# Kernel tuning notes

Measured on AMD Instinct MI355X. Metric: run time of the kernel, lower is better.

## Reference

```python
import jax, jax.numpy as jnp
import numpy as np

EPS = 1e-5

@jax.custom_vjp
def ste_quantize(w):
    # abs-mean scale, round, clamp to {-1, 0, 1}
    scale = jnp.maximum(jnp.mean(jnp.abs(w)), EPS)
    return jnp.clip(jnp.round(w / scale), -1.0, 1.0)

def _ste_fwd(w):
    return ste_quantize(w), None

def _ste_bwd(_, g):
    # straight-through: gradient passes unchanged
    return (g,)

ste_quantize.defvjp(_ste_fwd, _ste_bwd)


def setup_inputs() -> dict:
    key = jax.random.key(0)
    k1, k2 = jax.random.split(key)
    x = jax.random.normal(k1, (8, 8192, 1024), dtype=jnp.float32)       # [B, S, in]
    weight = jax.random.normal(k2, (1024, 1024), dtype=jnp.float32) * 0.02  # [out, in]
    return {"x": x, "weight": weight}


def reference(x, weight):
    w_ternary = ste_quantize(weight)                         # [out, in] in {-1,0,1}
    scale = jnp.maximum(jnp.mean(jnp.abs(weight)), EPS)      # scalar (differentiable path)
    # F.linear(x, w_ternary * scale): out = x @ (w_ternary*scale)^T
    return jnp.einsum('bsi,oi->bso', x, w_ternary * scale)
```

## Files before the change

### kernel.cpp

```cpp
#include <hip/hip_runtime.h>
#include <stdint.h>

#define K_DIM 1024
#define N_DIM 1024
#define M_MAX 65536

#define BM 256
#define BN 256
#define BK 32
#define NKT (K_DIM / BK)
#define NBUF 3
#define A_TILE (BM * BK)
#define B_TILE (BN * BK)

typedef __attribute__((ext_vector_type(8))) __bf16 bf16x8;
typedef __attribute__((ext_vector_type(4))) float f32x4;

__device__ __align__(16) unsigned short g_wq[N_DIM * K_DIM];
__device__ __align__(16) unsigned short g_xq[(size_t)M_MAX * K_DIM];
__device__ double g_partial[256];
__device__ float g_scale;

__device__ __forceinline__ unsigned int pack_bf16(float hi, float lo) {
  return __builtin_amdgcn_perm(__float_as_uint(hi), __float_as_uint(lo), 0x07060302u);
}

__global__ void absum_kernel(const float* __restrict__ w) {
  const int tid = threadIdx.x, bid = blockIdx.x;
  const float4* w4 = (const float4*)w;
  double s = 0.0;
#pragma unroll
  for (int i = 0; i < 4; i++) {
    float4 v = w4[bid * 1024 + i * 256 + tid];
    s += (double)fabsf(v.x) + (double)fabsf(v.y) + (double)fabsf(v.z) + (double)fabsf(v.w);
  }
#pragma unroll
  for (int o = 32; o > 0; o >>= 1) s += __shfl_down(s, o);
  __shared__ double sm[4];
  if ((tid & 63) == 0) sm[tid >> 6] = s;
  __syncthreads();
  if (tid == 0) g_partial[bid] = sm[0] + sm[1] + sm[2] + sm[3];
}

__global__ void scale_kernel() {
  const int tid = threadIdx.x;
  double v = g_partial[tid];
#pragma unroll
  for (int o = 32; o > 0; o >>= 1) v += __shfl_down(v, o);
  __shared__ double sm[4];
  if ((tid & 63) == 0) sm[tid >> 6] = v;
  __syncthreads();
  if (tid == 0) {
    double total = sm[0] + sm[1] + sm[2] + sm[3];
    double mean = total * (1.0 / 1048576.0);
    g_scale = (float)fmax(mean, 1e-5);
  }
}

__global__ void quant_kernel(const float* __restrict__ w) {
  const int idx = blockIdx.x * 256 + threadIdx.x;
  const float s = g_scale;
  float4 v = ((const float4*)w)[idx];
  float q0 = fminf(1.f, fmaxf(-1.f, rintf(v.x / s)));
  float q1 = fminf(1.f, fmaxf(-1.f, rintf(v.y / s)));
  float q2 = fminf(1.f, fmaxf(-1.f, rintf(v.z / s)));
  float q3 = fminf(1.f, fmaxf(-1.f, rintf(v.w / s)));
  ushort4 o;
  o.x = (unsigned short)(__float_as_uint(q0) >> 16);
  o.y = (unsigned short)(__float_as_uint(q1) >> 16);
  o.z = (unsigned short)(__float_as_uint(q2) >> 16);
  o.w = (unsigned short)(__float_as_uint(q3) >> 16);
  ((ushort4*)g_wq)[idx] = o;
}

__global__ __launch_bounds__(256) void convert_x(const float* __restrict__ x) {
  const size_t t = (size_t)blockIdx.x * 256 + threadIdx.x;
  const float4* x4 = (const float4*)x;
  float4 a = x4[t * 2];
  float4 b = x4[t * 2 + 1];
  uint4 o;
  o.x = pack_bf16(a.y, a.x);
  o.y = pack_bf16(a.w, a.z);
  o.z = pack_bf16(b.y, b.x);
  o.w = pack_bf16(b.w, b.z);
  ((uint4*)g_xq)[t] = o;
}

__global__ __launch_bounds__(512, 2) void bitlinear_gemm(float* __restrict__ C) {
  __shared__ __align__(16) unsigned short As[NBUF * A_TILE];
  __shared__ __align__(16) unsigned short Bs[NBUF * B_TILE];

  const int tid  = threadIdx.x;
  const int lane = tid & 63;
  const int wave = tid >> 6;
  const int wm   = wave >> 2;
  const int wn   = wave & 3;
  const int lm   = lane & 15;
  const int lq   = lane >> 4;

  const int b       = blockIdx.x;
  const int cpx     = (int)(gridDim.x >> 3);
  const int logical = (b & 7) * cpx + (b >> 3);
  const int mt      = logical >> 2;
  const int nt      = logical & 3;
  const int m0      = mt * BM;
  const int n0      = nt * BN;

  f32x4 acc[8][4];
#pragma unroll
  for (int i = 0; i < 8; i++)
#pragma unroll
    for (int j = 0; j < 4; j++) acc[i][j] = (f32x4){0.f, 0.f, 0.f, 0.f};

  const int cswz = ((lane & 3) ^ ((lane >> 3) & 3)) * 8;
  const unsigned short* aSrc =
      g_xq + (size_t)(m0 + wave * 32 + (lane >> 2)) * K_DIM + cswz;
  const unsigned short* bSrc =
      g_wq + (size_t)(n0 + wave * 32 + (lane >> 2)) * K_DIM + cswz;
  const int ldsDst = wave * 32 * BK;

#define STAGE_A(tt, bb)                                                        \
  do {                                                                         \
    const unsigned short* s_ = aSrc + (tt) * BK;                               \
    unsigned short* d_ = &As[(bb) * A_TILE + ldsDst];                          \
    __builtin_amdgcn_global_load_lds(                                          \
        (const __attribute__((address_space(1))) unsigned int*)s_,             \
        (__attribute__((address_space(3))) unsigned int*)d_, 16, 0, 0);        \
    __builtin_amdgcn_global_load_lds(                                          \
        (const __attribute__((address_space(1))) unsigned int*)(s_ + 16 * K_DIM), \
        (__attribute__((address_space(3))) unsigned int*)(d_ + 16 * BK), 16, 0, 0); \
  } while (0)

#define STAGE_B(tt, bb)                                                        \
  do {                                                                         \
    const unsigned short* s_ = bSrc + (tt) * BK;                               \
    unsigned short* d_ = &Bs[(bb) * B_TILE + ldsDst];                          \
    __builtin_amdgcn_global_load_lds(                                          \
        (const __attribute__((address_space(1))) unsigned int*)s_,             \
        (__attribute__((address_space(3))) unsigned int*)d_, 16, 0, 0);        \
    __builtin_amdgcn_global_load_lds(                                          \
        (const __attribute__((address_space(1))) unsigned int*)(s_ + 16 * K_DIM), \
        (__attribute__((address_space(3))) unsigned int*)(d_ + 16 * BK), 16, 0, 0); \
  } while (0)

  const int xorc = (((lm >> 1) & 3) ^ lq) * 8;
  const int aRd  = (wm * 128 + lm) * BK + xorc;
  const int bRd  = (wn * 64 + lm) * BK + xorc;

  STAGE_A(0, 0);
  STAGE_B(0, 0);
  STAGE_A(1, 1);
  STAGE_B(1, 1);

  int buf = 0;
#pragma unroll 1
  for (int t = 0; t < NKT; ++t) {
    if (t == NKT - 1)
      asm volatile("s_waitcnt vmcnt(0)\n\ts_barrier" ::: "memory");
    else
      asm volatile("s_waitcnt vmcnt(4)\n\ts_barrier" ::: "memory");

    const unsigned short* Ab = &As[buf * A_TILE + aRd];
    const unsigned short* Bb = &Bs[buf * B_TILE + bRd];
    const int nbuf = (buf + 2 >= NBUF) ? buf + 2 - NBUF : buf + 2;

    bf16x8 bfr[4], af[4];
#pragma unroll
    for (int nf = 0; nf < 4; ++nf) bfr[nf] = *(const bf16x8*)(Bb + nf * 16 * BK);
#pragma unroll
    for (int mf = 0; mf < 4; ++mf) af[mf] = *(const bf16x8*)(Ab + mf * 16 * BK);

    if (t + 2 < NKT) STAGE_A(t + 2, nbuf);

    __builtin_amdgcn_s_setprio(1);
#pragma unroll
    for (int mf = 0; mf < 4; ++mf)
#pragma unroll
      for (int nf = 0; nf < 4; ++nf)
        acc[mf][nf] = __builtin_amdgcn_mfma_f32_16x16x32_bf16(af[mf], bfr[nf],
                                                              acc[mf][nf], 0, 0, 0);
    __builtin_amdgcn_s_setprio(0);

    bf16x8 af2[4];
#pragma unroll
    for (int mf = 0; mf < 4; ++mf)
      af2[mf] = *(const bf16x8*)(Ab + (mf + 4) * 16 * BK);

    if (t + 2 < NKT) STAGE_B(t + 2, nbuf);

    __builtin_amdgcn_s_setprio(1);
#pragma unroll
    for (int mf = 0; mf < 4; ++mf)
#pragma unroll
      for (int nf = 0; nf < 4; ++nf)
        acc[mf + 4][nf] = __builtin_amdgcn_mfma_f32_16x16x32_bf16(
            af2[mf], bfr[nf], acc[mf + 4][nf], 0, 0, 0);
    __builtin_amdgcn_s_setprio(0);

    buf = (buf + 1 == NBUF) ? 0 : buf + 1;
  }
#undef STAGE_A
#undef STAGE_B

  const float s    = g_scale;
  const int   crow = m0 + wm * 128 + lq * 4;
  const int   ccol = n0 + wn * 64 + lm;
#pragma unroll
  for (int mf = 0; mf < 8; ++mf) {
#pragma unroll
    for (int nf = 0; nf < 4; ++nf) {
#pragma unroll
      for (int r = 0; r < 4; ++r) {
        C[(size_t)(crow + mf * 16 + r) * N_DIM + (ccol + nf * 16)] =
            acc[mf][nf][r] * s;
      }
    }
  }
}

extern "C" void kernel_launch(void* const* d_in, const int* in_sizes, int n_in,
                              void* d_out, int out_size, void* d_ws, size_t ws_size,
                              hipStream_t stream) {
  const float* x = (const float*)d_in[0];
  const float* w = (const float*)d_in[1];
  float* out = (float*)d_out;
  const int M = in_sizes[0] / K_DIM;

  hipLaunchKernelGGL(absum_kernel, dim3(256), dim3(256), 0, stream, w);
  hipLaunchKernelGGL(scale_kernel, dim3(1), dim3(256), 0, stream);
  hipLaunchKernelGGL(quant_kernel, dim3(1024), dim3(256), 0, stream, w);
  hipLaunchKernelGGL(convert_x, dim3((unsigned)((size_t)M * K_DIM / 8 / 256)), dim3(256), 0,
                     stream, x);
  hipLaunchKernelGGL(bitlinear_gemm,
                     dim3((unsigned)(((size_t)M / BM) * (N_DIM / BN))),
                     dim3(512), 0, stream, out);
}
```

Baseline: 620.0 us.

## Fuse fp32-to-bf16 conversion of x into GEMM A-tile loading

Removes the separate convert_x kernel and its 128MB bf16 intermediate buffer. The GEMM now loads fp32 x into registers one stage ahead, converts it to bf16 in-kernel, and writes it to LDS with a swizzle, reworking the pipeline waits and barriers around this. This saves a full read/write pass over x, but each x tile is now read as fp32 by every N-tile block (4 times), and the kernel takes on extra register pressure and conversion ALU work.

```diff
diff --git a/kernel.cpp b/kernel.cpp
--- a/kernel.cpp
+++ b/kernel.cpp
@@ -3,7 +3,6 @@
 
 #define K_DIM 1024
 #define N_DIM 1024
-#define M_MAX 65536
 
 #define BM 256
 #define BN 256
@@ -17,7 +16,6 @@
 typedef __attribute__((ext_vector_type(4))) float f32x4;
 
 __device__ __align__(16) unsigned short g_wq[N_DIM * K_DIM];
-__device__ __align__(16) unsigned short g_xq[(size_t)M_MAX * K_DIM];
 __device__ double g_partial[256];
 __device__ float g_scale;
 
@@ -73,20 +71,8 @@
   ((ushort4*)g_wq)[idx] = o;
 }
 
-__global__ __launch_bounds__(256) void convert_x(const float* __restrict__ x) {
-  const size_t t = (size_t)blockIdx.x * 256 + threadIdx.x;
-  const float4* x4 = (const float4*)x;
-  float4 a = x4[t * 2];
-  float4 b = x4[t * 2 + 1];
-  uint4 o;
-  o.x = pack_bf16(a.y, a.x);
-  o.y = pack_bf16(a.w, a.z);
-  o.z = pack_bf16(b.y, b.x);
-  o.w = pack_bf16(b.w, b.z);
-  ((uint4*)g_xq)[t] = o;
-}
-
-__global__ __launch_bounds__(512, 2) void bitlinear_gemm(float* __restrict__ C) {
+__global__ __launch_bounds__(512, 2) void bitlinear_gemm(const float* __restrict__ x,
+                                                         float* __restrict__ C) {
   __shared__ __align__(16) unsigned short As[NBUF * A_TILE];
   __shared__ __align__(16) unsigned short Bs[NBUF * B_TILE];
 
@@ -113,23 +99,9 @@
     for (int j = 0; j < 4; j++) acc[i][j] = (f32x4){0.f, 0.f, 0.f, 0.f};
 
   const int cswz = ((lane & 3) ^ ((lane >> 3) & 3)) * 8;
-  const unsigned short* aSrc =
-      g_xq + (size_t)(m0 + wave * 32 + (lane >> 2)) * K_DIM + cswz;
   const unsigned short* bSrc =
       g_wq + (size_t)(n0 + wave * 32 + (lane >> 2)) * K_DIM + cswz;
   const int ldsDst = wave * 32 * BK;
-
-#define STAGE_A(tt, bb)                                                        \
-  do {                                                                         \
-    const unsigned short* s_ = aSrc + (tt) * BK;                               \
-    unsigned short* d_ = &As[(bb) * A_TILE + ldsDst];                          \
-    __builtin_amdgcn_global_load_lds(                                          \
-        (const __attribute__((address_space(1))) unsigned int*)s_,             \
-        (__attribute__((address_space(3))) unsigned int*)d_, 16, 0, 0);        \
-    __builtin_amdgcn_global_load_lds(                                          \
-        (const __attribute__((address_space(1))) unsigned int*)(s_ + 16 * K_DIM), \
-        (__attribute__((address_space(3))) unsigned int*)(d_ + 16 * BK), 16, 0, 0); \
-  } while (0)
 
 #define STAGE_B(tt, bb)                                                        \
   do {                                                                         \
@@ -143,34 +115,69 @@
         (__attribute__((address_space(3))) unsigned int*)(d_ + 16 * BK), 16, 0, 0); \
   } while (0)
 
+  const int arow = wave * 32 + (lane >> 1);
+  const int ah   = lane & 1;
+  const int aswz = (lane >> 2) & 3;
+  const float4* aGlb =
+      (const float4*)(x + (size_t)(m0 + arow) * K_DIM + ah * 16);
+  const int wo0 = arow * BK + (((2 * ah) ^ aswz) * 8);
+  const int wo1 = arow * BK + (((2 * ah + 1) ^ aswz) * 8);
+
+  float4 aR0, aR1, aR2, aR3;
+
+#define LOAD_A(tt)                                                             \
+  do {                                                                         \
+    const float4* p_ = aGlb + (tt) * 8;                                        \
+    aR0 = p_[0]; aR1 = p_[1]; aR2 = p_[2]; aR3 = p_[3];                        \
+  } while (0)
+
+#define CVT_WRITE_A(bb)                                                        \
+  do {                                                                         \
+    uint4 p0_, p1_;                                                            \
+    p0_.x = pack_bf16(aR0.y, aR0.x); p0_.y = pack_bf16(aR0.w, aR0.z);          \
+    p0_.z = pack_bf16(aR1.y, aR1.x); p0_.w = pack_bf16(aR1.w, aR1.z);          \
+    p1_.x = pack_bf16(aR2.y, aR2.x); p1_.y = pack_bf16(aR2.w, aR2.z);          \
+    p1_.z = pack_bf16(aR3.y, aR3.x); p1_.w = pack_bf16(aR3.w, aR3.z);          \
+    *(uint4*)&As[(bb) * A_TILE + wo0] = p0_;                                   \
+    *(uint4*)&As[(bb) * A_TILE + wo1] = p1_;                                   \
+  } while (0)
+
   const int xorc = (((lm >> 1) & 3) ^ lq) * 8;
   const int aRd  = (wm * 128 + lm) * BK + xorc;
   const int bRd  = (wn * 64 + lm) * BK + xorc;
 
-  STAGE_A(0, 0);
-  STAGE_B(0, 0);
-  STAGE_A(1, 1);
-  STAGE_B(1, 1);
+  {
+    float4 t0, t1, t2, t3;
+    {
+      const float4* p_ = aGlb;
+      t0 = p_[0]; t1 = p_[1]; t2 = p_[2]; t3 = p_[3];
+    }
+    STAGE_B(0, 0);
+    LOAD_A(1);
+    STAGE_B(1, 1);
+    uint4 p0_, p1_;
+    p0_.x = pack_bf16(t0.y, t0.x); p0_.y = pack_bf16(t0.w, t0.z);
+    p0_.z = pack_bf16(t1.y, t1.x); p0_.w = pack_bf16(t1.w, t1.z);
+    p1_.x = pack_bf16(t2.y, t2.x); p1_.y = pack_bf16(t2.w, t2.z);
+    p1_.z = pack_bf16(t3.y, t3.x); p1_.w = pack_bf16(t3.w, t3.z);
+    *(uint4*)&As[wo0] = p0_;
+    *(uint4*)&As[wo1] = p1_;
+  }
+  asm volatile("s_waitcnt vmcnt(6) lgkmcnt(0)\n\ts_barrier" ::: "memory");
 
   int buf = 0;
 #pragma unroll 1
   for (int t = 0; t < NKT; ++t) {
-    if (t == NKT - 1)
-      asm volatile("s_waitcnt vmcnt(0)\n\ts_barrier" ::: "memory");
-    else
-      asm volatile("s_waitcnt vmcnt(4)\n\ts_barrier" ::: "memory");
-
     const unsigned short* Ab = &As[buf * A_TILE + aRd];
     const unsigned short* Bb = &Bs[buf * B_TILE + bRd];
     const int nbuf = (buf + 2 >= NBUF) ? buf + 2 - NBUF : buf + 2;
+    const int wbuf = (buf + 1 == NBUF) ? 0 : buf + 1;
 
     bf16x8 bfr[4], af[4];
 #pragma unroll
     for (int nf = 0; nf < 4; ++nf) bfr[nf] = *(const bf16x8*)(Bb + nf * 16 * BK);
 #pragma unroll
     for (int mf = 0; mf < 4; ++mf) af[mf] = *(const bf16x8*)(Ab + mf * 16 * BK);
-
-    if (t + 2 < NKT) STAGE_A(t + 2, nbuf);
 
     __builtin_amdgcn_s_setprio(1);
 #pragma unroll
@@ -186,7 +193,11 @@
     for (int mf = 0; mf < 4; ++mf)
       af2[mf] = *(const bf16x8*)(Ab + (mf + 4) * 16 * BK);
 
-    if (t + 2 < NKT) STAGE_B(t + 2, nbuf);
+    if (t < NKT - 1) CVT_WRITE_A(wbuf);
+    if (t < NKT - 2) {
+      LOAD_A(t + 2);
+      STAGE_B(t + 2, nbuf);
+    }
 
     __builtin_amdgcn_s_setprio(1);
 #pragma unroll
@@ -197,10 +208,16 @@
             af2[mf], bfr[nf], acc[mf + 4][nf], 0, 0, 0);
     __builtin_amdgcn_s_setprio(0);
 
-    buf = (buf + 1 == NBUF) ? 0 : buf + 1;
-  }
-#undef STAGE_A
+    if (t < NKT - 2)
+      asm volatile("s_waitcnt vmcnt(6) lgkmcnt(0)\n\ts_barrier" ::: "memory");
+    else if (t < NKT - 1)
+      asm volatile("s_waitcnt vmcnt(0) lgkmcnt(0)\n\ts_barrier" ::: "memory");
+
+    buf = wbuf;
+  }
 #undef STAGE_B
+#undef LOAD_A
+#undef CVT_WRITE_A
 
   const float s    = g_scale;
   const int   crow = m0 + wm * 128 + lq * 4;
@@ -229,9 +246,7 @@
   hipLaunchKernelGGL(absum_kernel, dim3(256), dim3(256), 0, stream, w);
   hipLaunchKernelGGL(scale_kernel, dim3(1), dim3(256), 0, stream);
   hipLaunchKernelGGL(quant_kernel, dim3(1024), dim3(256), 0, stream, w);
-  hipLaunchKernelGGL(convert_x, dim3((unsigned)((size_t)M * K_DIM / 8 / 256)), dim3(256), 0,
-                     stream, x);
   hipLaunchKernelGGL(bitlinear_gemm,
                      dim3((unsigned)(((size_t)M / BM) * (N_DIM / BN))),
-                     dim3(512), 0, stream, out);
-}
+                     dim3(512), 0, stream, x, out);
+}
```

Measured after the change: 565.9 us. 1.1x faster.
